# Kernel tuning notes

Hardware: AMD Instinct MI355X
Metric: run time of the kernel (lower is better)

Reference implementation:

```python
import jax, jax.numpy as jnp
import numpy as np

KH, KW = 3, 3
K_TERMS = KH * KW + 1  # ones (linear/bias) + 9 shifted patches
# pair indices (i<=j), same ordering as the original layer
_PAIRS = [(i, j) for i in range(K_TERMS) for j in range(i, K_TERMS)]
II = np.array([p[0] for p in _PAIRS])  # [55]
JJ = np.array([p[1] for p in _PAIRS])  # [55]


def setup_inputs() -> dict:
    key = jax.random.key(0)
    k1, k2 = jax.random.split(key)
    B, H, W, C, O = 8, 56, 56, 64, 128
    inputs = jax.random.normal(k1, (B, H, W, C), dtype=jnp.float32)
    # glorot-ish scale for the [1,1,55,C,O] conv3d kernel (squeezed to [55,C,O])
    fan = 55 * C + O
    kernel = jax.random.normal(k2, (55, C, O), dtype=jnp.float32) * jnp.sqrt(2.0 / fan)
    return {"inputs": inputs, "kernel": kernel}


def reference(inputs, kernel):
    B, H, W, C = inputs.shape
    # 'same' padding for stride 1: pad_total = k - 1, asymmetric split as in TF
    ph, pw = KH - 1, KW - 1
    xp = jnp.pad(inputs, ((0, 0), (ph // 2, ph - ph // 2), (pw // 2, pw - pw // 2), (0, 0)))
    # im2col-style shifted slices, row-major over (r, c) like i//kw, i%kw
    shifts = jnp.stack(
        [xp[:, r:r + H, c:c + W, :] for r in range(KH) for c in range(KW)],
        axis=3,
    )  # [B,H,W,9,C]
    ones = jnp.ones((B, H, W, 1, C), dtype=inputs.dtype)
    S = jnp.concatenate([ones, shifts], axis=3)  # [B,H,W,10,C]
    # pairwise quadratic features (includes bias = ones*ones and linear = ones*shift)
    quad = S[:, :, :, II, :] * S[:, :, :, JJ, :]  # [B,H,W,55,C]
    # 1x1x1 conv3d over depth-55 == contraction over (pair, channel)
    return jnp.einsum('bhwpc,pco->bhwo', quad, kernel)  # [B,H,W,O]
```

## Files before the change

### kernel.cpp

```cpp
#include <hip/hip_runtime.h>


#define CB 8
#define CH 56
#define CW 56
#define CC 64
#define CO 128
#define RS 72

typedef __attribute__((ext_vector_type(8))) _Float16 v8hf;
typedef __attribute__((ext_vector_type(16))) float f16f;
typedef __attribute__((address_space(3))) const _Float16 lds_cf16;

__device__ constexpr int PII[55] = {0,0,0,0,0,0,0,0,0,0, 1,1,1,1,1,1,1,1,1, 2,2,2,2,2,2,2,2,
                                    3,3,3,3,3,3,3, 4,4,4,4,4,4, 5,5,5,5,5, 6,6,6,6, 7,7,7, 8,8, 9};
__device__ constexpr int PJJ[55] = {0,1,2,3,4,5,6,7,8,9, 1,2,3,4,5,6,7,8,9, 2,3,4,5,6,7,8,9,
                                    3,4,5,6,7,8,9, 4,5,6,7,8,9, 5,6,7,8,9, 6,7,8,9, 7,8,9, 8,9, 9};

__global__ __launch_bounds__(256) void prep_kernel(const float* __restrict__ K,
                                                   _Float16* __restrict__ BtF) {
  __shared__ float tile[CC * CO];
  const int p = blockIdx.x;
  const int t = threadIdx.x;
  const float* src = K + (size_t)p * CC * CO;
#pragma unroll
  for (int e = 0; e < 8; ++e) {
    const int idx = t * 4 + e * 1024;
    *(float4*)&tile[idx] = *(const float4*)&src[idx];
  }
  __syncthreads();
#pragma unroll
  for (int e4 = 0; e4 < 4; ++e4) {
    const int idx = e4 * 256 + t;
    const int lane = idx & 63;
    const int nqq = (idx >> 6) & 3;
    const int ksq = idx >> 8;
    const int n = nqq * 32 + (lane & 31);
    const int kb = ksq * 16 + (lane >> 5) * 8;
    _Float16 ov[8];
#pragma unroll
    for (int e = 0; e < 8; ++e)
      ov[e] = (_Float16)tile[(kb + e) * CO + n];
    *(v8hf*)(BtF + ((size_t)p * 1024 + idx) * 8) = *(const v8hf*)ov;
  }
}

__global__ __launch_bounds__(256, 1) void quad_kernel(const float* __restrict__ in,
                                                      const _Float16* __restrict__ BtF,
                                                      float* __restrict__ out) {
  __shared__ _Float16 rowsH[3][64][RS];

  const int t = threadIdx.x;
  const int b = blockIdx.x / CH;
  const int hrow = blockIdx.x % CH;

  {
    const int col = t >> 2;
    const int cg = (t & 3) * 16;
    const int w = col - 1;
#pragma unroll
    for (int r = 0; r < 3; ++r) {
      const int hh = hrow + r - 1;
      const bool valid = (hh >= 0) && (hh < CH) && (w >= 0) && (w < CW);
      float4 v0 = make_float4(0.f, 0.f, 0.f, 0.f), v1 = v0, v2 = v0, v3 = v0;
      if (valid) {
        const float* s = in + (((size_t)(b * CH + hh)) * CW + w) * CC + cg;
        v0 = *(const float4*)(s);
        v1 = *(const float4*)(s + 4);
        v2 = *(const float4*)(s + 8);
        v3 = *(const float4*)(s + 12);
      }
      _Float16 pv[16];
      pv[0] = (_Float16)v0.x;  pv[1] = (_Float16)v0.y;  pv[2] = (_Float16)v0.z;  pv[3] = (_Float16)v0.w;
      pv[4] = (_Float16)v1.x;  pv[5] = (_Float16)v1.y;  pv[6] = (_Float16)v1.z;  pv[7] = (_Float16)v1.w;
      pv[8] = (_Float16)v2.x;  pv[9] = (_Float16)v2.y;  pv[10] = (_Float16)v2.z; pv[11] = (_Float16)v2.w;
      pv[12] = (_Float16)v3.x; pv[13] = (_Float16)v3.y; pv[14] = (_Float16)v3.z; pv[15] = (_Float16)v3.w;
      _Float16* d = &rowsH[r][col][cg];
      *(v8hf*)(d) = *(const v8hf*)&pv[0];
      *(v8hf*)(d + 8) = *(const v8hf*)&pv[8];
    }
  }

  const int lane = t & 63;
  const int nq = t >> 6;
  const int ml = lane & 31;
  const int hk = lane >> 5;
  const int h8 = hk * 8;

  f16f acc0, acc1;
#pragma unroll
  for (int r = 0; r < 16; ++r) { acc0[r] = 0.f; acc1[r] = 0.f; }

  const _Float16* Bw = BtF + (size_t)(nq * 64 + lane) * 8;
  const v8hf vone = {1, 1, 1, 1, 1, 1, 1, 1};

  lds_cf16* lds3 = (lds_cf16*)&rowsH[0][0][0];

  v8hf ring[11];
#pragma unroll
  for (int p = 0; p < 11; ++p) {
    const _Float16* ba = Bw + (size_t)p * 8192;
    asm volatile("global_load_dwordx4 %0, %1, off" : "=v"(ring[p]) : "v"(ba));
  }

  __syncthreads();

#pragma unroll 1
  for (int ks = 0; ks < 4; ++ks) {
    const int koff = ks * 16 + h8;
    v8hf s0[9], s1[9];
#pragma unroll
    for (int tt = 0; tt < 9; ++tt) {
      const int rr = tt / 3, sc = tt % 3;
      const int c0 = ml + sc;
      int c1 = 32 + ml + sc; c1 = c1 > 63 ? 63 : c1;
      lds_cf16* p0 = lds3 + (rr * 64 + c0) * RS + koff;
      lds_cf16* p1 = lds3 + (rr * 64 + c1) * RS + koff;
      asm volatile("ds_read_b128 %0, %1" : "=v"(s0[tt]) : "v"(p0));
      asm volatile("ds_read_b128 %0, %1" : "=v"(s1[tt]) : "v"(p1));
    }
    asm volatile("s_waitcnt lgkmcnt(0)"
                 : "+v"(s0[0]), "+v"(s0[1]), "+v"(s0[2]), "+v"(s0[3]), "+v"(s0[4]),
                   "+v"(s0[5]), "+v"(s0[6]), "+v"(s0[7]), "+v"(s0[8]),
                   "+v"(s1[0]), "+v"(s1[1]), "+v"(s1[2]), "+v"(s1[3]), "+v"(s1[4]),
                   "+v"(s1[5]), "+v"(s1[6]), "+v"(s1[7]), "+v"(s1[8]));

    const int ksn = (ks < 3) ? ks + 1 : 3;
#pragma unroll
    for (int p = 0; p < 55; ++p) {
      asm volatile("s_waitcnt vmcnt(10)" : "+v"(ring[p % 11]));
      const v8hf bb = ring[p % 11];
      {
        const int p2 = (p < 44) ? p + 11 : p - 44;
        const int ks2 = (p < 44) ? ks : ksn;
        const _Float16* ba = Bw + (size_t)p2 * 8192 + ks2 * 2048;
        asm volatile("global_load_dwordx4 %0, %1, off" : "=v"(ring[p % 11]) : "v"(ba));
      }
      const int pi = PII[p], pj = PJJ[p];
      v8hf a0, a1;
      if (pi == 0) {
        if (pj == 0) { a0 = vone; a1 = vone; }
        else { a0 = s0[pj - 1]; a1 = s1[pj - 1]; }
      } else {
        a0 = s0[pi - 1] * s0[pj - 1];
        a1 = s1[pi - 1] * s1[pj - 1];
      }
      acc0 = __builtin_amdgcn_mfma_f32_32x32x16_f16(a0, bb, acc0, 0, 0, 0);
      acc1 = __builtin_amdgcn_mfma_f32_32x32x16_f16(a1, bb, acc1, 0, 0, 0);
    }
  }
  asm volatile("s_waitcnt vmcnt(0)");

  float* ob = out + ((size_t)(b * CH + hrow) * CW) * CO + nq * 32 + ml;
#pragma unroll
  for (int r = 0; r < 16; ++r) {
    const int wp = (r & 3) + 8 * (r >> 2) + 4 * hk;
    ob[(size_t)wp * CO] = acc0[r];
  }
#pragma unroll
  for (int r = 0; r < 12; ++r) {
    const int wp = 32 + (r & 3) + 8 * (r >> 2) + 4 * hk;
    ob[(size_t)wp * CO] = acc1[r];
  }
}

extern "C" void kernel_launch(void* const* d_in, const int* in_sizes, int n_in,
                              void* d_out, int out_size, void* d_ws, size_t ws_size,
                              hipStream_t stream) {
  const float* in = (const float*)d_in[0];
  const float* K = (const float*)d_in[1];
  float* out = (float*)d_out;
  _Float16* BtF = (_Float16*)d_ws;
  (void)in_sizes; (void)n_in; (void)out_size; (void)ws_size;

  prep_kernel<<<55, 256, 0, stream>>>(K, BtF);
  quad_kernel<<<CB * CH, 256, 0, stream>>>(in, BtF, out);
}
```

Before: 89.93 us.

## Compute two output rows per block to reuse weight loads and halo rows

Each block now processes two adjacent output rows instead of one. It loads four input rows into LDS, which shares the halo, and issues four MFMAs per weight fragment instead of two. This halves global weight traffic per output and halves the grid size. The cost is more registers for accumulators and patches, and with 224 blocks on a 256-CU device some CUs sit idle.

```diff
diff --git a/kernel.cpp b/kernel.cpp
--- a/kernel.cpp
+++ b/kernel.cpp
@@ -48,19 +48,19 @@
 __global__ __launch_bounds__(256, 1) void quad_kernel(const float* __restrict__ in,
                                                       const _Float16* __restrict__ BtF,
                                                       float* __restrict__ out) {
-  __shared__ _Float16 rowsH[3][64][RS];
+  __shared__ _Float16 rowsH[4][64][RS];
 
   const int t = threadIdx.x;
-  const int b = blockIdx.x / CH;
-  const int hrow = blockIdx.x % CH;
+  const int b = blockIdx.x / (CH / 2);
+  const int h0 = (blockIdx.x % (CH / 2)) * 2;
 
   {
     const int col = t >> 2;
     const int cg = (t & 3) * 16;
     const int w = col - 1;
 #pragma unroll
-    for (int r = 0; r < 3; ++r) {
-      const int hh = hrow + r - 1;
+    for (int r = 0; r < 4; ++r) {
+      const int hh = h0 + r - 1;
       const bool valid = (hh >= 0) && (hh < CH) && (w >= 0) && (w < CW);
       float4 v0 = make_float4(0.f, 0.f, 0.f, 0.f), v1 = v0, v2 = v0, v3 = v0;
       if (valid) {
@@ -87,9 +87,9 @@
   const int hk = lane >> 5;
   const int h8 = hk * 8;
 
-  f16f acc0, acc1;
+  f16f acc00, acc01, acc10, acc11;
 #pragma unroll
-  for (int r = 0; r < 16; ++r) { acc0[r] = 0.f; acc1[r] = 0.f; }
+  for (int r = 0; r < 16; ++r) { acc00[r] = 0.f; acc01[r] = 0.f; acc10[r] = 0.f; acc11[r] = 0.f; }
 
   const _Float16* Bw = BtF + (size_t)(nq * 64 + lane) * 8;
   const v8hf vone = {1, 1, 1, 1, 1, 1, 1, 1};
@@ -108,22 +108,25 @@
 #pragma unroll 1
   for (int ks = 0; ks < 4; ++ks) {
     const int koff = ks * 16 + h8;
-    v8hf s0[9], s1[9];
+    v8hf sv0[12], sv1[12];
 #pragma unroll
-    for (int tt = 0; tt < 9; ++tt) {
-      const int rr = tt / 3, sc = tt % 3;
-      const int c0 = ml + sc;
-      int c1 = 32 + ml + sc; c1 = c1 > 63 ? 63 : c1;
-      lds_cf16* p0 = lds3 + (rr * 64 + c0) * RS + koff;
-      lds_cf16* p1 = lds3 + (rr * 64 + c1) * RS + koff;
-      asm volatile("ds_read_b128 %0, %1" : "=v"(s0[tt]) : "v"(p0));
-      asm volatile("ds_read_b128 %0, %1" : "=v"(s1[tt]) : "v"(p1));
-    }
+    for (int rr = 0; rr < 4; ++rr)
+#pragma unroll
+      for (int dx = 0; dx < 3; ++dx) {
+        const int c0 = ml + dx;
+        int c1 = 32 + ml + dx; c1 = c1 > 63 ? 63 : c1;
+        lds_cf16* p0 = lds3 + (rr * 64 + c0) * RS + koff;
+        lds_cf16* p1 = lds3 + (rr * 64 + c1) * RS + koff;
+        asm volatile("ds_read_b128 %0, %1" : "=v"(sv0[rr * 3 + dx]) : "v"(p0));
+        asm volatile("ds_read_b128 %0, %1" : "=v"(sv1[rr * 3 + dx]) : "v"(p1));
+      }
     asm volatile("s_waitcnt lgkmcnt(0)"
-                 : "+v"(s0[0]), "+v"(s0[1]), "+v"(s0[2]), "+v"(s0[3]), "+v"(s0[4]),
-                   "+v"(s0[5]), "+v"(s0[6]), "+v"(s0[7]), "+v"(s0[8]),
-                   "+v"(s1[0]), "+v"(s1[1]), "+v"(s1[2]), "+v"(s1[3]), "+v"(s1[4]),
-                   "+v"(s1[5]), "+v"(s1[6]), "+v"(s1[7]), "+v"(s1[8]));
+                 : "+v"(sv0[0]), "+v"(sv0[1]), "+v"(sv0[2]), "+v"(sv0[3]),
+                   "+v"(sv0[4]), "+v"(sv0[5]), "+v"(sv0[6]), "+v"(sv0[7]),
+                   "+v"(sv0[8]), "+v"(sv0[9]), "+v"(sv0[10]), "+v"(sv0[11]),
+                   "+v"(sv1[0]), "+v"(sv1[1]), "+v"(sv1[2]), "+v"(sv1[3]),
+                   "+v"(sv1[4]), "+v"(sv1[5]), "+v"(sv1[6]), "+v"(sv1[7]),
+                   "+v"(sv1[8]), "+v"(sv1[9]), "+v"(sv1[10]), "+v"(sv1[11]));
 
     const int ksn = (ks < 3) ? ks + 1 : 3;
 #pragma unroll
@@ -137,30 +140,45 @@
         asm volatile("global_load_dwordx4 %0, %1, off" : "=v"(ring[p % 11]) : "v"(ba));
       }
       const int pi = PII[p], pj = PJJ[p];
-      v8hf a0, a1;
+      v8hf a00, a01, a10, a11;
       if (pi == 0) {
-        if (pj == 0) { a0 = vone; a1 = vone; }
-        else { a0 = s0[pj - 1]; a1 = s1[pj - 1]; }
+        if (pj == 0) { a00 = vone; a01 = vone; a10 = vone; a11 = vone; }
+        else {
+          const int dy = (pj - 1) / 3, dx = (pj - 1) % 3;
+          a00 = sv0[dy * 3 + dx];        a01 = sv1[dy * 3 + dx];
+          a10 = sv0[(dy + 1) * 3 + dx];  a11 = sv1[(dy + 1) * 3 + dx];
+        }
       } else {
-        a0 = s0[pi - 1] * s0[pj - 1];
-        a1 = s1[pi - 1] * s1[pj - 1];
+        const int dyi = (pi - 1) / 3, dxi = (pi - 1) % 3;
+        const int dyj = (pj - 1) / 3, dxj = (pj - 1) % 3;
+        a00 = sv0[dyi * 3 + dxi] * sv0[dyj * 3 + dxj];
+        a01 = sv1[dyi * 3 + dxi] * sv1[dyj * 3 + dxj];
+        a10 = sv0[(dyi + 1) * 3 + dxi] * sv0[(dyj + 1) * 3 + dxj];
+        a11 = sv1[(dyi + 1) * 3 + dxi] * sv1[(dyj + 1) * 3 + dxj];
       }
-      acc0 = __builtin_amdgcn_mfma_f32_32x32x16_f16(a0, bb, acc0, 0, 0, 0);
-      acc1 = __builtin_amdgcn_mfma_f32_32x32x16_f16(a1, bb, acc1, 0, 0, 0);
+      acc00 = __builtin_amdgcn_mfma_f32_32x32x16_f16(a00, bb, acc00, 0, 0, 0);
+      acc01 = __builtin_amdgcn_mfma_f32_32x32x16_f16(a01, bb, acc01, 0, 0, 0);
+      acc10 = __builtin_amdgcn_mfma_f32_32x32x16_f16(a10, bb, acc10, 0, 0, 0);
+      acc11 = __builtin_amdgcn_mfma_f32_32x32x16_f16(a11, bb, acc11, 0, 0, 0);
     }
   }
   asm volatile("s_waitcnt vmcnt(0)");
 
-  float* ob = out + ((size_t)(b * CH + hrow) * CW) * CO + nq * 32 + ml;
 #pragma unroll
-  for (int r = 0; r < 16; ++r) {
-    const int wp = (r & 3) + 8 * (r >> 2) + 4 * hk;
-    ob[(size_t)wp * CO] = acc0[r];
-  }
+  for (int rw = 0; rw < 2; ++rw) {
+    float* ob = out + ((size_t)(b * CH + h0 + rw) * CW) * CO + nq * 32 + ml;
+    const f16f accc0 = rw ? acc10 : acc00;
+    const f16f accc1 = rw ? acc11 : acc01;
 #pragma unroll
-  for (int r = 0; r < 12; ++r) {
-    const int wp = 32 + (r & 3) + 8 * (r >> 2) + 4 * hk;
-    ob[(size_t)wp * CO] = acc1[r];
+    for (int r = 0; r < 16; ++r) {
+      const int wp = (r & 3) + 8 * (r >> 2) + 4 * hk;
+      ob[(size_t)wp * CO] = accc0[r];
+    }
+#pragma unroll
+    for (int r = 0; r < 12; ++r) {
+      const int wp = 32 + (r & 3) + 8 * (r >> 2) + 4 * hk;
+      ob[(size_t)wp * CO] = accc1[r];
+    }
   }
 }
 
@@ -174,5 +192,5 @@
   (void)in_sizes; (void)n_in; (void)out_size; (void)ws_size;
 
   prep_kernel<<<55, 256, 0, stream>>>(K, BtF);
-  quad_kernel<<<CB * CH, 256, 0, stream>>>(in, BtF, out);
+  quad_kernel<<<CB * (CH / 2), 256, 0, stream>>>(in, BtF, out);
 }
```

Result: faster. 86.18 us (-4.2%).
